# Kernel optimization log

Hardware: AMD Instinct MI355X
Metric: run time of the kernel (lower is better)

## Reference

```python
import jax, jax.numpy as jnp
import numpy as np
from jax import lax

B, S, I = 128, 256, 128          # batch, seq_len, input_size
CTX, OUT = 256, 128              # context_input_size, output_size
CPM, NM = 1024, 4                # center_size_per_module, num_modules
CENTER = NM * CPM
IN_SIZES = [I + CTX, CTX, CTX, CTX]          # only module 0 sees the input
HID = [CPM, CPM, CPM, CPM + OUT]             # last module also emits output


def setup_inputs() -> dict:
    key = jax.random.key(0)
    ks = jax.random.split(key, 4 + 5 * NM)
    d = {
        "inputs": jax.random.normal(ks[0], (B, 1, S, I), jnp.float32),
        "center_init": jax.random.normal(ks[1], (NM, B, CPM), jnp.float32),
        "mod_init": jax.random.normal(ks[2], (NM - 1, B, CPM), jnp.float32),
        "mod_init_last": jax.random.normal(ks[3], (B, CPM + OUT), jnp.float32),
    }
    for i in range(NM):
        k = ks[4 + 5 * i: 4 + 5 * (i + 1)]
        d[f"pm{i}"] = jax.random.normal(k[0], (CENTER, CTX), jnp.float32) * 0.02
        d[f"wih{i}"] = jax.random.normal(k[1], (3 * HID[i], IN_SIZES[i]), jnp.float32) * 0.05
        d[f"whh{i}"] = jax.random.normal(k[2], (3 * HID[i], HID[i]), jnp.float32) * 0.05
        d[f"bih{i}"] = jnp.zeros((3 * HID[i],), jnp.float32)
        d[f"bhh{i}"] = jnp.zeros((3 * HID[i],), jnp.float32)
    return d


def _gru(x, h, wih, whh, bih, bhh):
    # PyTorch GRUCell semantics
    gi = x @ wih.T + bih
    gh = h @ whh.T + bhh
    ir, iz, inn = jnp.split(gi, 3, axis=1)
    hr, hz, hn = jnp.split(gh, 3, axis=1)
    r = jax.nn.sigmoid(ir + hr)
    z = jax.nn.sigmoid(iz + hz)
    n = jnp.tanh(inn + r * hn)
    return (1.0 - z) * n + z * h


def _forward(inputs, center_init, mod_init, mod_init_last, pms, wihs, whhs, bihs, bhhs):
    xs = jnp.swapaxes(inputs[:, 0], 0, 1)  # [S, B, I]

    def step(carry, x_t):
        centers, mods, mod_last = carry  # [NM,B,CPM], [NM-1,B,CPM], [B,CPM+OUT]
        # torch.cat(prev_center_states, dim=1): module-major concat -> [B, NM*CPM]
        center_state = jnp.reshape(jnp.swapaxes(centers, 0, 1), (centers.shape[1], -1))
        new_centers, new_mods = [], []
        out = new_mod_last = None
        for i in range(NM):
            ctx = center_state @ pms[i]                       # [B, CTX]
            xin = jnp.concatenate([x_t, ctx], axis=1) if i == 0 else ctx
            h_prev = mod_last if i == NM - 1 else mods[i]
            h = _gru(xin, h_prev, wihs[i], whhs[i], bihs[i], bhhs[i])
            if i == NM - 1:
                out = h[:, :OUT]                              # split([output, center_feat])
                new_centers.append(h[:, OUT:])
                new_mod_last = h
            else:
                new_centers.append(h)
                new_mods.append(h)
        return (jnp.stack(new_centers), jnp.stack(new_mods), new_mod_last), out

    _, ys = lax.scan(step, (center_init, mod_init, mod_init_last), xs)
    return jnp.swapaxes(ys, 0, 1)  # [B, S, OUT]


def reference(inputs, center_init, mod_init, mod_init_last,
              pm0, pm1, pm2, pm3,
              wih0, wih1, wih2, wih3,
              whh0, whh1, whh2, whh3,
              bih0, bih1, bih2, bih3,
              bhh0, bhh1, bhh2, bhh3):
    return _forward(inputs, center_init, mod_init, mod_init_last,
                    (pm0, pm1, pm2, pm3),
                    (wih0, wih1, wih2, wih3),
                    (whh0, whh1, whh2, whh3),
                    (bih0, bih1, bih2, bih3),
                    (bhh0, bhh1, bhh2, bhh3))
```

## Files before the change

### kernel.cpp

```cpp
#include <hip/hip_runtime.h>
#include <hip/hip_bf16.h>

typedef _Float16 f16;
typedef f16  f16x8 __attribute__((ext_vector_type(8)));
typedef float f32x4 __attribute__((ext_vector_type(4)));

__device__ __forceinline__ f16x8 ld8h(const f16* p){ return *reinterpret_cast<const f16x8*>(p); }
__device__ __forceinline__ void fsplit(float x, f16* hi, f16* lo){
    f16 h=(f16)x; *hi=h; *lo=(f16)((x-(float)h)*4096.0f);
}
#define MFMA16(a,b,c) __builtin_amdgcn_mfma_f32_16x16x32_f16((a),(b),(c),0,0,0)
__device__ __forceinline__ size_t fragoff(int n, int k, int Kc){
    return ((size_t)(n>>4)*Kc + (k>>5))*512 + (size_t)((((k&31)>>3)*16 + (n&15))*8 + (k&7));
}

constexpr size_t NXE   = 128ull*256*128;
constexpr size_t NPM   = 1024ull*4096;
constexpr size_t NWIH0 = 3072ull*384;
constexpr size_t NWIH12= 3072ull*256;
constexpr size_t NWIH3 = 3456ull*256;
constexpr size_t NWHH  = 3072ull*1024;
constexpr size_t NWHH3 = 3456ull*1152;
constexpr size_t NCTX  = 128ull*1024;
constexpr size_t NHMX  = 128ull*1152;

constexpr size_t OFF_XH    = 0;
constexpr size_t OFF_XL    = OFF_XH + NXE*2;
constexpr size_t OFF_PMH   = OFF_XL + NXE*2;
constexpr size_t OFF_PML   = OFF_PMH + NPM*2;
constexpr size_t OFF_WIHH0 = OFF_PML + NPM*2;
constexpr size_t OFF_WIHH1 = OFF_WIHH0 + NWIH0*2;
constexpr size_t OFF_WIHH2 = OFF_WIHH1 + NWIH12*2;
constexpr size_t OFF_WIHH3 = OFF_WIHH2 + NWIH12*2;
constexpr size_t OFF_WIHL0 = OFF_WIHH3 + NWIH3*2;
constexpr size_t OFF_WIHL1 = OFF_WIHL0 + NWIH0*2;
constexpr size_t OFF_WIHL2 = OFF_WIHL1 + NWIH12*2;
constexpr size_t OFF_WIHL3 = OFF_WIHL2 + NWIH12*2;
constexpr size_t OFF_WHHH0 = OFF_WIHL3 + NWIH3*2;
constexpr size_t OFF_WHHH1 = OFF_WHHH0 + NWHH*2;
constexpr size_t OFF_WHHH2 = OFF_WHHH1 + NWHH*2;
constexpr size_t OFF_WHHH3 = OFF_WHHH2 + NWHH*2;
constexpr size_t OFF_WHHL0 = OFF_WHHH3 + NWHH3*2;
constexpr size_t OFF_WHHL1 = OFF_WHHL0 + NWHH*2;
constexpr size_t OFF_WHHL2 = OFF_WHHL1 + NWHH*2;
constexpr size_t OFF_WHHL3 = OFF_WHHL2 + NWHH*2;
constexpr size_t OFF_C0H   = OFF_WHHL3 + NWHH3*2;
constexpr size_t OFF_C0L   = OFF_C0H + 4*NHMX*2;
constexpr size_t OFF_CTXH  = OFF_C0L + 4*NHMX*2;
constexpr size_t OFF_CTXL  = OFF_CTXH + NCTX*2;
constexpr size_t OFF_HH    = OFF_CTXL + NCTX*2;
constexpr size_t OFF_HL    = OFF_HH + 8*NHMX*2;
constexpr size_t WS_NEED   = OFF_HL + 8*NHMX*2;

__device__ __forceinline__ f16* hh_ptr(char* ws,int p,int i){ return (f16*)(ws+OFF_HH+((size_t)(p*4+i))*NHMX*2); }
__device__ __forceinline__ f16* hl_ptr(char* ws,int p,int i){ return (f16*)(ws+OFF_HL+((size_t)(p*4+i))*NHMX*2); }

__global__ void k_repack_w(const float* __restrict__ src, f16* __restrict__ hi,
                           f16* __restrict__ lo, int K){
    int n = blockIdx.x;
    const float* row = src + (size_t)n*K;
    int Kc = K >> 5;
    for (int k8 = threadIdx.x*8; k8 < K; k8 += 2048) {
        f16x8 hv, lv;
        #pragma unroll
        for (int e = 0; e < 8; ++e) { f16 a,b; fsplit(row[k8+e], &a, &b); hv[e]=a; lv[e]=b; }
        size_t d = fragoff(n, k8, Kc);
        *reinterpret_cast<f16x8*>(hi + d) = hv;
        *reinterpret_cast<f16x8*>(lo + d) = lv;
    }
}

__global__ void k_repack_pm(const float* __restrict__ p0, const float* __restrict__ p1,
                            const float* __restrict__ p2, const float* __restrict__ p3,
                            f16* __restrict__ hi, f16* __restrict__ lo){
    int k0 = blockIdx.x * 8;
    for (int c = threadIdx.x; c < 1024; c += 256) {
        int i = c >> 8, nl = c & 255;
        const float* p = (i==0?p0 : i==1?p1 : i==2?p2 : p3);
        #pragma unroll
        for (int e = 0; e < 8; ++e) {
            f16 a,b; fsplit(p[(size_t)(k0+e)*256 + nl], &a, &b);
            size_t d = fragoff(c, k0+e, 128); hi[d]=a; lo[d]=b;
        }
    }
}

__global__ void k_repack_x(const float* __restrict__ src, f16* __restrict__ hi, f16* __restrict__ lo){
    size_t g = ((size_t)blockIdx.x*256 + threadIdx.x) * 8;
    if (g >= NXE) return;
    int m = (int)(g >> 15), t = (int)((g >> 7) & 255), d0 = (int)(g & 127);
    f16x8 hv, lv;
    #pragma unroll
    for (int e = 0; e < 8; ++e) { f16 a,b; fsplit(src[g+e], &a, &b); hv[e]=a; lv[e]=b; }
    size_t d = (size_t)t*16384 + fragoff(m, d0, 4);
    *reinterpret_cast<f16x8*>(hi + d) = hv;
    *reinterpret_cast<f16x8*>(lo + d) = lv;
}

__global__ void k_init_cen(const float* __restrict__ ci, char* ws){
    size_t g = ((size_t)blockIdx.x*256 + threadIdx.x) * 8;
    if (g >= 4ull*128*1024) return;
    int i = (int)(g >> 17), b = (int)((g >> 10) & 127), c = (int)(g & 1023);
    f16* hi = (f16*)(ws + OFF_C0H) + (size_t)i*NHMX;
    f16* lo = (f16*)(ws + OFF_C0L) + (size_t)i*NHMX;
    f16x8 hv, lv;
    #pragma unroll
    for (int e = 0; e < 8; ++e) { f16 a,bb; fsplit(ci[g+e], &a, &bb); hv[e]=a; lv[e]=bb; }
    size_t d = (i < 3) ? fragoff(b, c, 32) : fragoff(b, 128 + c, 36);
    *reinterpret_cast<f16x8*>(hi + d) = hv;
    *reinterpret_cast<f16x8*>(lo + d) = lv;
}

__global__ void k_init_mod(const float* __restrict__ mi, char* ws){
    size_t g = ((size_t)blockIdx.x*256 + threadIdx.x) * 8;
    if (g >= 3ull*128*1024) return;
    int i = (int)(g >> 17), b = (int)((g >> 10) & 127), j = (int)(g & 1023);
    f16 *hh = hh_ptr(ws, 0, i), *hl = hl_ptr(ws, 0, i);
    f16x8 hv, lv;
    #pragma unroll
    for (int e = 0; e < 8; ++e) { f16 a,bb; fsplit(mi[g+e], &a, &bb); hv[e]=a; lv[e]=bb; }
    size_t d = fragoff(b, j, 32);
    *reinterpret_cast<f16x8*>(hh + d) = hv;
    *reinterpret_cast<f16x8*>(hl + d) = lv;
}

__global__ void k_init_last(const float* __restrict__ ml, char* ws){
    int b = blockIdx.x;
    f16 *hh = hh_ptr(ws, 0, 3), *hl = hl_ptr(ws, 0, 3);
    for (int j = threadIdx.x*8; j < 1152; j += 2048) {
        f16x8 hv, lv;
        #pragma unroll
        for (int e = 0; e < 8; ++e) { f16 a,bb; fsplit(ml[(size_t)b*1152 + j + e], &a, &bb); hv[e]=a; lv[e]=bb; }
        size_t d = fragoff(b, j, 36);
        *reinterpret_cast<f16x8*>(hh + d) = hv;
        *reinterpret_cast<f16x8*>(hl + d) = lv;
    }
}

__global__ __launch_bounds__(512) void k_ctx(char* ws, int par, int t){
    __shared__ float red[8][32][17];
    const f16* pmh  = (const f16*)(ws + OFF_PMH);
    const f16* pml  = (const f16*)(ws + OFF_PML);
    int tid = threadIdx.x, lane = tid & 63, wv = tid >> 6;
    int bm = blockIdx.x >> 6, bn = blockIdx.x & 63;
    int mod = wv >> 1, half = wv & 1;
    const int Kc_m = (mod == 3) ? 36 : 32;
    const int koff = ((mod == 3) ? 4 : 0) + half*16;
    const f16 *Ah, *Al;
    if (t == 0) {
        Ah = (const f16*)(ws + OFF_C0H) + (size_t)mod*NHMX;
        Al = (const f16*)(ws + OFF_C0L) + (size_t)mod*NHMX;
    } else {
        Ah = hh_ptr(ws, par, mod);
        Al = hl_ptr(ws, par, mod);
    }
    size_t lb = (size_t)lane*8;
    size_t a0 = ((size_t)(bm*2)*Kc_m + koff)*512 + lb;
    size_t a1 = a0 + (size_t)Kc_m*512;
    size_t bb = ((size_t)bn*128 + wv*16)*512 + lb;
    f32x4 h0={},h1={},c0={},c1={};
    #pragma unroll 4
    for (int kc = 0; kc < 16; ++kc) {
        f16x8 bh = ld8h(pmh + bb + kc*512), bl = ld8h(pml + bb + kc*512);
        f16x8 ah0 = ld8h(Ah + a0 + kc*512), al0 = ld8h(Al + a0 + kc*512);
        f16x8 ah1 = ld8h(Ah + a1 + kc*512), al1 = ld8h(Al + a1 + kc*512);
        h0 = MFMA16(ah0,bh,h0); c0 = MFMA16(al0,bh,c0); c0 = MFMA16(ah0,bl,c0);
        h1 = MFMA16(ah1,bh,h1); c1 = MFMA16(al1,bh,c1); c1 = MFMA16(ah1,bl,c1);
    }
    int rg = lane >> 4, fr = lane & 15;
    const float inv = 1.0f/4096.0f;
    #pragma unroll
    for (int rr = 0; rr < 4; ++rr) {
        red[wv][rg*4+rr][fr]      = h0[rr] + c0[rr]*inv;
        red[wv][16+rg*4+rr][fr]   = h1[rr] + c1[rr]*inv;
    }
    __syncthreads();
    int r = tid >> 4, c = tid & 15;
    float s = red[0][r][c]+red[1][r][c]+red[2][r][c]+red[3][r][c]
            + red[4][r][c]+red[5][r][c]+red[6][r][c]+red[7][r][c];
    int m = bm*32 + r, n = bn*16 + c;
    size_t d = fragoff(m, n, 32);
    f16* ctxh = (f16*)(ws + OFF_CTXH);
    f16* ctxl = (f16*)(ws + OFF_CTXL);
    fsplit(s, &ctxh[d], &ctxl[d]);
}

__global__ __launch_bounds__(512, 2) void k_fused(char* ws,
    const float* __restrict__ bih0, const float* __restrict__ bih1,
    const float* __restrict__ bih2, const float* __restrict__ bih3,
    const float* __restrict__ bhh0, const float* __restrict__ bhh1,
    const float* __restrict__ bhh2, const float* __restrict__ bhh3,
    float* __restrict__ out, int t, int par)
{
    __shared__ float red[3][4][64][17];
    const int tid = threadIdx.x, lane = tid & 63, wv = tid >> 6;
    const int kq = wv & 3, mp = wv >> 2;
    const int fr = lane & 15, rg = lane >> 4;
    const int tile = blockIdx.x >> 1, rh = blockIdx.x & 1;
    int i, jt;
    if (tile < 64)       { i = 0; jt = tile; }
    else if (tile < 128) { i = 1; jt = tile - 64; }
    else if (tile < 192) { i = 2; jt = tile - 128; }
    else                 { i = 3; jt = tile - 192; }
    const int H  = (i == 3) ? 1152 : 1024;
    const int K1 = (i == 0) ? 384 : 256;
    const int Kc1 = K1 >> 5, KcH = H >> 5, Ht = H >> 4;
    const int P1q = Kc1 >> 2, PHq = KcH >> 2;

    const f16* WihH = (const f16*)(ws + (i==0?OFF_WIHH0 : i==1?OFF_WIHH1 : i==2?OFF_WIHH2 : OFF_WIHH3));
    const f16* WihL = (const f16*)(ws + (i==0?OFF_WIHL0 : i==1?OFF_WIHL1 : i==2?OFF_WIHL2 : OFF_WIHL3));
    const f16* WhhH = (const f16*)(ws + (i==0?OFF_WHHH0 : i==1?OFF_WHHH1 : i==2?OFF_WHHH2 : OFF_WHHH3));
    const f16* WhhL = (const f16*)(ws + (i==0?OFF_WHHL0 : i==1?OFF_WHHL1 : i==2?OFF_WHHL2 : OFF_WHHL3));

    const size_t lb = (size_t)lane*8;
    size_t b1[3], b2[3];
    #pragma unroll
    for (int s = 0; s < 3; ++s) {
        b1[s] = ((size_t)(s*Ht + jt)*Kc1)*512 + lb;
        b2[s] = ((size_t)(s*Ht + jt)*KcH)*512 + lb;
    }
    const int mt0 = rh*4 + mp*2;

    f32x4 aRh[2]={{},{}}, aRc[2]={{},{}}, aZh[2]={{},{}}, aZc[2]={{},{}};
    f32x4 aIh[2]={{},{}}, aIc[2]={{},{}}, aNh[2]={{},{}}, aNc[2]={{},{}};

    {
        const f16* XH_ = (const f16*)(ws + OFF_XH);
        const f16* XL_ = (const f16*)(ws + OFF_XL);
        const f16* CH_ = (const f16*)(ws + OFF_CTXH);
        const f16* CL_ = (const f16*)(ws + OFF_CTXL);
        size_t xb0 = ((size_t)(t*8 + mt0)*4)*512 + lb, xb1 = xb0 + 2048;
        size_t cb0 = ((size_t)mt0*32)*512 + lb,        cb1 = cb0 + 16384;
        const int kc0 = kq*P1q, kc1e = kc0 + P1q;
        #pragma unroll 2
        for (int kc = kc0; kc < kc1e; ++kc) {
            f16x8 ah0, al0, ah1, al1;
            if (i == 0 && kc < 4) {
                ah0 = ld8h(XH_ + xb0 + kc*512); al0 = ld8h(XL_ + xb0 + kc*512);
                ah1 = ld8h(XH_ + xb1 + kc*512); al1 = ld8h(XL_ + xb1 + kc*512);
            } else {
                const int ck = (i == 0) ? kc - 4 : i*8 + kc;
                ah0 = ld8h(CH_ + cb0 + ck*512); al0 = ld8h(CL_ + cb0 + ck*512);
                ah1 = ld8h(CH_ + cb1 + ck*512); al1 = ld8h(CL_ + cb1 + ck*512);
            }
            f16x8 bh, bl;
            bh = ld8h(WihH + b1[0] + kc*512); bl = ld8h(WihL + b1[0] + kc*512);
            aRh[0]=MFMA16(ah0,bh,aRh[0]); aRc[0]=MFMA16(al0,bh,aRc[0]); aRc[0]=MFMA16(ah0,bl,aRc[0]);
            aRh[1]=MFMA16(ah1,bh,aRh[1]); aRc[1]=MFMA16(al1,bh,aRc[1]); aRc[1]=MFMA16(ah1,bl,aRc[1]);
            bh = ld8h(WihH + b1[1] + kc*512); bl = ld8h(WihL + b1[1] + kc*512);
            aZh[0]=MFMA16(ah0,bh,aZh[0]); aZc[0]=MFMA16(al0,bh,aZc[0]); aZc[0]=MFMA16(ah0,bl,aZc[0]);
            aZh[1]=MFMA16(ah1,bh,aZh[1]); aZc[1]=MFMA16(al1,bh,aZc[1]); aZc[1]=MFMA16(ah1,bl,aZc[1]);
            bh = ld8h(WihH + b1[2] + kc*512); bl = ld8h(WihL + b1[2] + kc*512);
            aIh[0]=MFMA16(ah0,bh,aIh[0]); aIc[0]=MFMA16(al0,bh,aIc[0]); aIc[0]=MFMA16(ah0,bl,aIc[0]);
            aIh[1]=MFMA16(ah1,bh,aIh[1]); aIc[1]=MFMA16(al1,bh,aIc[1]); aIc[1]=MFMA16(ah1,bl,aIc[1]);
        }
    }
    {
        const f16* HHp = hh_ptr(ws, par, i);
        const f16* HLp = hl_ptr(ws, par, i);
        size_t hb0 = ((size_t)mt0*KcH)*512 + lb, hb1 = hb0 + (size_t)KcH*512;
        const int kc0 = kq*PHq, kc1e = kc0 + PHq;
        #pragma unroll 2
        for (int kc = kc0; kc < kc1e; ++kc) {
            f16x8 ah0 = ld8h(HHp + hb0 + kc*512), al0 = ld8h(HLp + hb0 + kc*512);
            f16x8 ah1 = ld8h(HHp + hb1 + kc*512), al1 = ld8h(HLp + hb1 + kc*512);
            f16x8 bh, bl;
            bh = ld8h(WhhH + b2[0] + kc*512); bl = ld8h(WhhL + b2[0] + kc*512);
            aRh[0]=MFMA16(ah0,bh,aRh[0]); aRc[0]=MFMA16(al0,bh,aRc[0]); aRc[0]=MFMA16(ah0,bl,aRc[0]);
            aRh[1]=MFMA16(ah1,bh,aRh[1]); aRc[1]=MFMA16(al1,bh,aRc[1]); aRc[1]=MFMA16(ah1,bl,aRc[1]);
            bh = ld8h(WhhH + b2[1] + kc*512); bl = ld8h(WhhL + b2[1] + kc*512);
            aZh[0]=MFMA16(ah0,bh,aZh[0]); aZc[0]=MFMA16(al0,bh,aZc[0]); aZc[0]=MFMA16(ah0,bl,aZc[0]);
            aZh[1]=MFMA16(ah1,bh,aZh[1]); aZc[1]=MFMA16(al1,bh,aZc[1]); aZc[1]=MFMA16(ah1,bl,aZc[1]);
            bh = ld8h(WhhH + b2[2] + kc*512); bl = ld8h(WhhL + b2[2] + kc*512);
            aNh[0]=MFMA16(ah0,bh,aNh[0]); aNc[0]=MFMA16(al0,bh,aNc[0]); aNc[0]=MFMA16(ah0,bl,aNc[0]);
            aNh[1]=MFMA16(ah1,bh,aNh[1]); aNc[1]=MFMA16(al1,bh,aNc[1]); aNc[1]=MFMA16(ah1,bl,aNc[1]);
        }
    }

    const float inv = 1.0f/4096.0f;
    const int r16 = rg*4;
    if (kq != 0) {
        #pragma unroll
        for (int mi = 0; mi < 2; ++mi) {
            #pragma unroll
            for (int rr = 0; rr < 4; ++rr) {
                const int row = mp*32 + mi*16 + r16 + rr;
                red[kq-1][0][row][fr] = aRh[mi][rr] + aRc[mi][rr]*inv;
                red[kq-1][1][row][fr] = aZh[mi][rr] + aZc[mi][rr]*inv;
                red[kq-1][2][row][fr] = aIh[mi][rr] + aIc[mi][rr]*inv;
                red[kq-1][3][row][fr] = aNh[mi][rr] + aNc[mi][rr]*inv;
            }
        }
    }
    __syncthreads();
    if (kq != 0) return;

    const float* bihp = (i==0?bih0 : i==1?bih1 : i==2?bih2 : bih3);
    const float* bhhp = (i==0?bhh0 : i==1?bhh1 : i==2?bhh2 : bhh3);
    const int j = jt*16 + fr;
    const float bir = bihp[j], biz = bihp[H+j], bin = bihp[2*H+j];
    const float bhr = bhhp[j], bhz = bhhp[H+j], bhn = bhhp[2*H+j];
    const f16* hhP = hh_ptr(ws, par, i);
    const f16* hlP = hl_ptr(ws, par, i);
    f16 *hhN = hh_ptr(ws, par^1, i), *hlN = hl_ptr(ws, par^1, i);
    #pragma unroll
    for (int mi = 0; mi < 2; ++mi) {
        #pragma unroll
        for (int rr = 0; rr < 4; ++rr) {
            const int row = mp*32 + mi*16 + r16 + rr;
            float r_  = aRh[mi][rr] + aRc[mi][rr]*inv
                      + red[0][0][row][fr] + red[1][0][row][fr] + red[2][0][row][fr] + bir + bhr;
            float z_  = aZh[mi][rr] + aZc[mi][rr]*inv
                      + red[0][1][row][fr] + red[1][1][row][fr] + red[2][1][row][fr] + biz + bhz;
            float in_ = aIh[mi][rr] + aIc[mi][rr]*inv
                      + red[0][2][row][fr] + red[1][2][row][fr] + red[2][2][row][fr] + bin;
            float hn_ = aNh[mi][rr] + aNc[mi][rr]*inv
                      + red[0][3][row][fr] + red[1][3][row][fr] + red[2][3][row][fr] + bhn;
            float rgt = 1.f/(1.f + expf(-r_));
            float zgt = 1.f/(1.f + expf(-z_));
            float ngt = tanhf(in_ + rgt*hn_);
            const int m = rh*64 + row;
            size_t hd = fragoff(m, j, KcH);
            float hp = (float)hhP[hd] + (float)hlP[hd]*inv;
            float hnew = (1.f - zgt)*ngt + zgt*hp;
            fsplit(hnew, &hhN[hd], &hlN[hd]);
            if (i == 3 && j < 128)
                out[((size_t)m*256 + t)*128 + j] = hnew;
        }
    }
}

extern "C" void kernel_launch(void* const* d_in, const int* in_sizes, int n_in,
                              void* d_out, int out_size, void* d_ws, size_t ws_size,
                              hipStream_t stream)
{
    char* ws = (char*)d_ws;
    const float* inp   = (const float*)d_in[0];
    const float* cini  = (const float*)d_in[1];
    const float* mini  = (const float*)d_in[2];
    const float* mlast = (const float*)d_in[3];
    const float *pm[4], *wih[4], *whh[4], *bih[4], *bhh[4];
    for (int i = 0; i < 4; ++i) {
        pm[i]  = (const float*)d_in[4 + 5*i];
        wih[i] = (const float*)d_in[5 + 5*i];
        whh[i] = (const float*)d_in[6 + 5*i];
        bih[i] = (const float*)d_in[7 + 5*i];
        bhh[i] = (const float*)d_in[8 + 5*i];
    }
    float* out = (float*)d_out;

    k_repack_x<<<2048, 256, 0, stream>>>(inp, (f16*)(ws+OFF_XH), (f16*)(ws+OFF_XL));
    k_repack_pm<<<512, 256, 0, stream>>>(pm[0], pm[1], pm[2], pm[3],
                                         (f16*)(ws+OFF_PMH), (f16*)(ws+OFF_PML));
    k_repack_w<<<3072, 256, 0, stream>>>(wih[0], (f16*)(ws+OFF_WIHH0), (f16*)(ws+OFF_WIHL0), 384);
    k_repack_w<<<3072, 256, 0, stream>>>(wih[1], (f16*)(ws+OFF_WIHH1), (f16*)(ws+OFF_WIHL1), 256);
    k_repack_w<<<3072, 256, 0, stream>>>(wih[2], (f16*)(ws+OFF_WIHH2), (f16*)(ws+OFF_WIHL2), 256);
    k_repack_w<<<3456, 256, 0, stream>>>(wih[3], (f16*)(ws+OFF_WIHH3), (f16*)(ws+OFF_WIHL3), 256);
    k_repack_w<<<3072, 256, 0, stream>>>(whh[0], (f16*)(ws+OFF_WHHH0), (f16*)(ws+OFF_WHHL0), 1024);
    k_repack_w<<<3072, 256, 0, stream>>>(whh[1], (f16*)(ws+OFF_WHHH1), (f16*)(ws+OFF_WHHL1), 1024);
    k_repack_w<<<3072, 256, 0, stream>>>(whh[2], (f16*)(ws+OFF_WHHH2), (f16*)(ws+OFF_WHHL2), 1024);
    k_repack_w<<<3456, 256, 0, stream>>>(whh[3], (f16*)(ws+OFF_WHHH3), (f16*)(ws+OFF_WHHL3), 1152);
    k_init_cen<<<256, 256, 0, stream>>>(cini, ws);
    k_init_mod<<<192, 256, 0, stream>>>(mini, ws);
    k_init_last<<<128, 256, 0, stream>>>(mlast, ws);

    for (int t = 0; t < 256; ++t) {
        int par = t & 1;
        k_ctx<<<256, 512, 0, stream>>>(ws, par, t);
        k_fused<<<528, 512, 0, stream>>>(ws,
            bih[0], bih[1], bih[2], bih[3],
            bhh[0], bhh[1], bhh[2], bhh[3],
            out, t, par);
    }
    (void)in_sizes; (void)n_in; (void)out_size; (void)ws_size; (void)WS_NEED;
}
```

Before: 12.58 ms.

## Run recurrent W_hh GEMM concurrently with context GEMM in one launch

The recurrent h@W_hh^T product no longer depends on the context, so it moves into a combined kernel that runs alongside the context GEMM blocks. Its gate pre-activations are written to a new global scratch buffer. A second kernel then computes only the input-side GEMM and the GRU elementwise update, reading those values back. The aim is to shorten the serial critical path per timestep and use more CUs at once, at the cost of an extra global round trip for the gate values and a reworked tile schedule with blocks interleaved by stride 66.

After: 13.66 ms. 1.09x slower.

```diff
diff --git a/kernel.cpp b/kernel.cpp
--- a/kernel.cpp
+++ b/kernel.cpp
@@ -50,7 +50,8 @@
 constexpr size_t OFF_CTXL  = OFF_CTXH + NCTX*2;
 constexpr size_t OFF_HH    = OFF_CTXL + NCTX*2;
 constexpr size_t OFF_HL    = OFF_HH + 8*NHMX*2;
-constexpr size_t WS_NEED   = OFF_HL + 8*NHMX*2;
+constexpr size_t OFF_G2    = OFF_HL + 8*NHMX*2;
+constexpr size_t WS_NEED   = OFF_G2 + 528ull*3*1024*4;
 
 __device__ __forceinline__ f16* hh_ptr(char* ws,int p,int i){ return (f16*)(ws+OFF_HH+((size_t)(p*4+i))*NHMX*2); }
 __device__ __forceinline__ f16* hl_ptr(char* ws,int p,int i){ return (f16*)(ws+OFF_HL+((size_t)(p*4+i))*NHMX*2); }
@@ -137,66 +138,147 @@
     }
 }
 
-__global__ __launch_bounds__(512) void k_ctx(char* ws, int par, int t){
-    __shared__ float red[8][32][17];
-    const f16* pmh  = (const f16*)(ws + OFF_PMH);
-    const f16* pml  = (const f16*)(ws + OFF_PML);
-    int tid = threadIdx.x, lane = tid & 63, wv = tid >> 6;
-    int bm = blockIdx.x >> 6, bn = blockIdx.x & 63;
-    int mod = wv >> 1, half = wv & 1;
-    const int Kc_m = (mod == 3) ? 36 : 32;
-    const int koff = ((mod == 3) ? 4 : 0) + half*16;
-    const f16 *Ah, *Al;
-    if (t == 0) {
-        Ah = (const f16*)(ws + OFF_C0H) + (size_t)mod*NHMX;
-        Al = (const f16*)(ws + OFF_C0L) + (size_t)mod*NHMX;
-    } else {
-        Ah = hh_ptr(ws, par, mod);
-        Al = hl_ptr(ws, par, mod);
-    }
-    size_t lb = (size_t)lane*8;
-    size_t a0 = ((size_t)(bm*2)*Kc_m + koff)*512 + lb;
-    size_t a1 = a0 + (size_t)Kc_m*512;
-    size_t bb = ((size_t)bn*128 + wv*16)*512 + lb;
-    f32x4 h0={},h1={},c0={},c1={};
-    #pragma unroll 4
-    for (int kc = 0; kc < 16; ++kc) {
-        f16x8 bh = ld8h(pmh + bb + kc*512), bl = ld8h(pml + bb + kc*512);
-        f16x8 ah0 = ld8h(Ah + a0 + kc*512), al0 = ld8h(Al + a0 + kc*512);
-        f16x8 ah1 = ld8h(Ah + a1 + kc*512), al1 = ld8h(Al + a1 + kc*512);
-        h0 = MFMA16(ah0,bh,h0); c0 = MFMA16(al0,bh,c0); c0 = MFMA16(ah0,bl,c0);
-        h1 = MFMA16(ah1,bh,h1); c1 = MFMA16(al1,bh,c1); c1 = MFMA16(ah1,bl,c1);
-    }
-    int rg = lane >> 4, fr = lane & 15;
+__global__ __launch_bounds__(512, 2) void k_union(char* ws, int t, int par)
+{
+    __shared__ float smem[9792];
+    const int tid = threadIdx.x, lane = tid & 63, wv = tid >> 6;
+    const int fr = lane & 15, rg = lane >> 4;
+    const size_t lb = (size_t)lane*8;
     const float inv = 1.0f/4096.0f;
-    #pragma unroll
-    for (int rr = 0; rr < 4; ++rr) {
-        red[wv][rg*4+rr][fr]      = h0[rr] + c0[rr]*inv;
-        red[wv][16+rg*4+rr][fr]   = h1[rr] + c1[rr]*inv;
+
+    if (blockIdx.x < 256) {
+        float (*red)[32][17] = (float(*)[32][17])smem;
+        const f16* pmh  = (const f16*)(ws + OFF_PMH);
+        const f16* pml  = (const f16*)(ws + OFF_PML);
+        int bm = blockIdx.x >> 6, bn = blockIdx.x & 63;
+        int mod = wv >> 1, half = wv & 1;
+        const int Kc_m = (mod == 3) ? 36 : 32;
+        const int koff = ((mod == 3) ? 4 : 0) + half*16;
+        const f16 *Ah, *Al;
+        if (t == 0) {
+            Ah = (const f16*)(ws + OFF_C0H) + (size_t)mod*NHMX;
+            Al = (const f16*)(ws + OFF_C0L) + (size_t)mod*NHMX;
+        } else {
+            Ah = hh_ptr(ws, par, mod);
+            Al = hl_ptr(ws, par, mod);
+        }
+        size_t a0 = ((size_t)(bm*2)*Kc_m + koff)*512 + lb;
+        size_t a1 = a0 + (size_t)Kc_m*512;
+        size_t bb = ((size_t)bn*128 + wv*16)*512 + lb;
+        f32x4 h0={},h1={},c0={},c1={};
+        #pragma unroll 4
+        for (int kc = 0; kc < 16; ++kc) {
+            f16x8 bh = ld8h(pmh + bb + kc*512), bl = ld8h(pml + bb + kc*512);
+            f16x8 ah0 = ld8h(Ah + a0 + kc*512), al0 = ld8h(Al + a0 + kc*512);
+            f16x8 ah1 = ld8h(Ah + a1 + kc*512), al1 = ld8h(Al + a1 + kc*512);
+            h0 = MFMA16(ah0,bh,h0); c0 = MFMA16(al0,bh,c0); c0 = MFMA16(ah0,bl,c0);
+            h1 = MFMA16(ah1,bh,h1); c1 = MFMA16(al1,bh,c1); c1 = MFMA16(ah1,bl,c1);
+        }
+        #pragma unroll
+        for (int rr = 0; rr < 4; ++rr) {
+            red[wv][rg*4+rr][fr]    = h0[rr] + c0[rr]*inv;
+            red[wv][16+rg*4+rr][fr] = h1[rr] + c1[rr]*inv;
+        }
+        __syncthreads();
+        int r = tid >> 4, c = tid & 15;
+        float s = red[0][r][c]+red[1][r][c]+red[2][r][c]+red[3][r][c]
+                + red[4][r][c]+red[5][r][c]+red[6][r][c]+red[7][r][c];
+        int m = bm*32 + r, n = bn*16 + c;
+        size_t d = fragoff(m, n, 32);
+        f16* ctxh = (f16*)(ws + OFF_CTXH);
+        f16* ctxl = (f16*)(ws + OFF_CTXL);
+        fsplit(s, &ctxh[d], &ctxl[d]);
+        return;
+    }
+
+    float (*red)[3][64][17] = (float(*)[3][64][17])smem;
+    const int hid = blockIdx.x - 256;
+    const int lid = (hid & 7)*66 + (hid >> 3);
+    const int tile = lid >> 1, rh = lid & 1;
+    int i, jt;
+    if (tile < 64)       { i = 0; jt = tile; }
+    else if (tile < 128) { i = 1; jt = tile - 64; }
+    else if (tile < 192) { i = 2; jt = tile - 128; }
+    else                 { i = 3; jt = tile - 192; }
+    const int H  = (i == 3) ? 1152 : 1024;
+    const int KcH = H >> 5, Ht = H >> 4;
+    const int PHq = KcH >> 2;
+
+    const f16* WhhH = (const f16*)(ws + (i==0?OFF_WHHH0 : i==1?OFF_WHHH1 : i==2?OFF_WHHH2 : OFF_WHHH3));
+    const f16* WhhL = (const f16*)(ws + (i==0?OFF_WHHL0 : i==1?OFF_WHHL1 : i==2?OFF_WHHL2 : OFF_WHHL3));
+    size_t b2[3];
+    #pragma unroll
+    for (int s = 0; s < 3; ++s) b2[s] = ((size_t)(s*Ht + jt)*KcH)*512 + lb;
+
+    const int kq = wv & 3, mp = wv >> 2;
+    const int mt0 = rh*4 + mp*2;
+    f32x4 aRh[2]={{},{}}, aRc[2]={{},{}}, aZh[2]={{},{}}, aZc[2]={{},{}};
+    f32x4 aNh[2]={{},{}}, aNc[2]={{},{}};
+
+    const f16* HHp = hh_ptr(ws, par, i);
+    const f16* HLp = hl_ptr(ws, par, i);
+    size_t hb0 = ((size_t)mt0*KcH)*512 + lb, hb1 = hb0 + (size_t)KcH*512;
+    const int kc0 = kq*PHq, kc1e = kc0 + PHq;
+    #pragma unroll 2
+    for (int kc = kc0; kc < kc1e; ++kc) {
+        f16x8 ah0 = ld8h(HHp + hb0 + kc*512), al0 = ld8h(HLp + hb0 + kc*512);
+        f16x8 ah1 = ld8h(HHp + hb1 + kc*512), al1 = ld8h(HLp + hb1 + kc*512);
+        f16x8 bh, bl;
+        bh = ld8h(WhhH + b2[0] + kc*512); bl = ld8h(WhhL + b2[0] + kc*512);
+        aRh[0]=MFMA16(ah0,bh,aRh[0]); aRc[0]=MFMA16(al0,bh,aRc[0]); aRc[0]=MFMA16(ah0,bl,aRc[0]);
+        aRh[1]=MFMA16(ah1,bh,aRh[1]); aRc[1]=MFMA16(al1,bh,aRc[1]); aRc[1]=MFMA16(ah1,bl,aRc[1]);
+        bh = ld8h(WhhH + b2[1] + kc*512); bl = ld8h(WhhL + b2[1] + kc*512);
+        aZh[0]=MFMA16(ah0,bh,aZh[0]); aZc[0]=MFMA16(al0,bh,aZc[0]); aZc[0]=MFMA16(ah0,bl,aZc[0]);
+        aZh[1]=MFMA16(ah1,bh,aZh[1]); aZc[1]=MFMA16(al1,bh,aZc[1]); aZc[1]=MFMA16(ah1,bl,aZc[1]);
+        bh = ld8h(WhhH + b2[2] + kc*512); bl = ld8h(WhhL + b2[2] + kc*512);
+        aNh[0]=MFMA16(ah0,bh,aNh[0]); aNc[0]=MFMA16(al0,bh,aNc[0]); aNc[0]=MFMA16(ah0,bl,aNc[0]);
+        aNh[1]=MFMA16(ah1,bh,aNh[1]); aNc[1]=MFMA16(al1,bh,aNc[1]); aNc[1]=MFMA16(ah1,bl,aNc[1]);
+    }
+
+    const int r16 = rg*4;
+    if (kq != 0) {
+        #pragma unroll
+        for (int mi = 0; mi < 2; ++mi) {
+            #pragma unroll
+            for (int rr = 0; rr < 4; ++rr) {
+                const int row = mp*32 + mi*16 + r16 + rr;
+                red[kq-1][0][row][fr] = aRh[mi][rr] + aRc[mi][rr]*inv;
+                red[kq-1][1][row][fr] = aZh[mi][rr] + aZc[mi][rr]*inv;
+                red[kq-1][2][row][fr] = aNh[mi][rr] + aNc[mi][rr]*inv;
+            }
+        }
     }
     __syncthreads();
-    int r = tid >> 4, c = tid & 15;
-    float s = red[0][r][c]+red[1][r][c]+red[2][r][c]+red[3][r][c]
-            + red[4][r][c]+red[5][r][c]+red[6][r][c]+red[7][r][c];
-    int m = bm*32 + r, n = bn*16 + c;
-    size_t d = fragoff(m, n, 32);
-    f16* ctxh = (f16*)(ws + OFF_CTXH);
-    f16* ctxl = (f16*)(ws + OFF_CTXL);
-    fsplit(s, &ctxh[d], &ctxl[d]);
-}
-
-__global__ __launch_bounds__(512, 2) void k_fused(char* ws,
+    if (kq != 0) return;
+
+    float* G2 = (float*)(ws + OFF_G2) + (size_t)lid*3*1024;
+    #pragma unroll
+    for (int mi = 0; mi < 2; ++mi) {
+        #pragma unroll
+        for (int rr = 0; rr < 4; ++rr) {
+            const int row = mp*32 + mi*16 + r16 + rr;
+            float R = aRh[mi][rr] + aRc[mi][rr]*inv + red[0][0][row][fr] + red[1][0][row][fr] + red[2][0][row][fr];
+            float Z = aZh[mi][rr] + aZc[mi][rr]*inv + red[0][1][row][fr] + red[1][1][row][fr] + red[2][1][row][fr];
+            float N = aNh[mi][rr] + aNc[mi][rr]*inv + red[0][2][row][fr] + red[1][2][row][fr] + red[2][2][row][fr];
+            G2[0*1024 + row*16 + fr] = R;
+            G2[1*1024 + row*16 + fr] = Z;
+            G2[2*1024 + row*16 + fr] = N;
+        }
+    }
+}
+
+__global__ __launch_bounds__(256, 2) void k_rest(char* ws,
     const float* __restrict__ bih0, const float* __restrict__ bih1,
     const float* __restrict__ bih2, const float* __restrict__ bih3,
     const float* __restrict__ bhh0, const float* __restrict__ bhh1,
     const float* __restrict__ bhh2, const float* __restrict__ bhh3,
     float* __restrict__ out, int t, int par)
 {
-    __shared__ float red[3][4][64][17];
-    const int tid = threadIdx.x, lane = tid & 63, wv = tid >> 6;
-    const int kq = wv & 3, mp = wv >> 2;
+    __shared__ float red[3][3][64][17];
+    const int tid = threadIdx.x, lane = tid & 63, kq = tid >> 6;
     const int fr = lane & 15, rg = lane >> 4;
-    const int tile = blockIdx.x >> 1, rh = blockIdx.x & 1;
+    const int lid = (blockIdx.x & 7)*66 + (blockIdx.x >> 3);
+    const int tile = lid >> 1, rh = lid & 1;
     int i, jt;
     if (tile < 64)       { i = 0; jt = tile; }
     else if (tile < 128) { i = 1; jt = tile - 64; }
@@ -204,76 +286,58 @@
     else                 { i = 3; jt = tile - 192; }
     const int H  = (i == 3) ? 1152 : 1024;
     const int K1 = (i == 0) ? 384 : 256;
-    const int Kc1 = K1 >> 5, KcH = H >> 5, Ht = H >> 4;
-    const int P1q = Kc1 >> 2, PHq = KcH >> 2;
+    const int Kc1 = K1 >> 5, Ht = H >> 4;
+    const int KcH = H >> 5;
+    const int P1q = Kc1 >> 2;
 
     const f16* WihH = (const f16*)(ws + (i==0?OFF_WIHH0 : i==1?OFF_WIHH1 : i==2?OFF_WIHH2 : OFF_WIHH3));
     const f16* WihL = (const f16*)(ws + (i==0?OFF_WIHL0 : i==1?OFF_WIHL1 : i==2?OFF_WIHL2 : OFF_WIHL3));
-    const f16* WhhH = (const f16*)(ws + (i==0?OFF_WHHH0 : i==1?OFF_WHHH1 : i==2?OFF_WHHH2 : OFF_WHHH3));
-    const f16* WhhL = (const f16*)(ws + (i==0?OFF_WHHL0 : i==1?OFF_WHHL1 : i==2?OFF_WHHL2 : OFF_WHHL3));
-
     const size_t lb = (size_t)lane*8;
-    size_t b1[3], b2[3];
-    #pragma unroll
-    for (int s = 0; s < 3; ++s) {
-        b1[s] = ((size_t)(s*Ht + jt)*Kc1)*512 + lb;
-        b2[s] = ((size_t)(s*Ht + jt)*KcH)*512 + lb;
-    }
-    const int mt0 = rh*4 + mp*2;
-
-    f32x4 aRh[2]={{},{}}, aRc[2]={{},{}}, aZh[2]={{},{}}, aZc[2]={{},{}};
-    f32x4 aIh[2]={{},{}}, aIc[2]={{},{}}, aNh[2]={{},{}}, aNc[2]={{},{}};
+    size_t b1[3];
+    #pragma unroll
+    for (int s = 0; s < 3; ++s) b1[s] = ((size_t)(s*Ht + jt)*Kc1)*512 + lb;
+    const int mt0 = rh*4;
+
+    f32x4 aRh[4]={}, aRc[4]={}, aZh[4]={}, aZc[4]={}, aIh[4]={}, aIc[4]={};
 
     {
         const f16* XH_ = (const f16*)(ws + OFF_XH);
         const f16* XL_ = (const f16*)(ws + OFF_XL);
         const f16* CH_ = (const f16*)(ws + OFF_CTXH);
         const f16* CL_ = (const f16*)(ws + OFF_CTXL);
-        size_t xb0 = ((size_t)(t*8 + mt0)*4)*512 + lb, xb1 = xb0 + 2048;
-        size_t cb0 = ((size_t)mt0*32)*512 + lb,        cb1 = cb0 + 16384;
+        size_t xb[4], cb[4];
+        #pragma unroll
+        for (int f = 0; f < 4; ++f) {
+            xb[f] = ((size_t)(t*8 + mt0 + f)*4)*512 + lb;
+            cb[f] = ((size_t)(mt0 + f)*32)*512 + lb;
+        }
         const int kc0 = kq*P1q, kc1e = kc0 + P1q;
-        #pragma unroll 2
         for (int kc = kc0; kc < kc1e; ++kc) {
-            f16x8 ah0, al0, ah1, al1;
+            f16x8 ah[4], al[4];
             if (i == 0 && kc < 4) {
-                ah0 = ld8h(XH_ + xb0 + kc*512); al0 = ld8h(XL_ + xb0 + kc*512);
-                ah1 = ld8h(XH_ + xb1 + kc*512); al1 = ld8h(XL_ + xb1 + kc*512);
+                #pragma unroll
+                for (int f = 0; f < 4; ++f) { ah[f] = ld8h(XH_ + xb[f] + kc*512); al[f] = ld8h(XL_ + xb[f] + kc*512); }
             } else {
                 const int ck = (i == 0) ? kc - 4 : i*8 + kc;
-                ah0 = ld8h(CH_ + cb0 + ck*512); al0 = ld8h(CL_ + cb0 + ck*512);
-                ah1 = ld8h(CH_ + cb1 + ck*512); al1 = ld8h(CL_ + cb1 + ck*512);
+                #pragma unroll
+                for (int f = 0; f < 4; ++f) { ah[f] = ld8h(CH_ + cb[f] + ck*512); al[f] = ld8h(CL_ + cb[f] + ck*512); }
             }
             f16x8 bh, bl;
             bh = ld8h(WihH + b1[0] + kc*512); bl = ld8h(WihL + b1[0] + kc*512);
-            aRh[0]=MFMA16(ah0,bh,aRh[0]); aRc[0]=MFMA16(al0,bh,aRc[0]); aRc[0]=MFMA16(ah0,bl,aRc[0]);
-            aRh[1]=MFMA16(ah1,bh,aRh[1]); aRc[1]=MFMA16(al1,bh,aRc[1]); aRc[1]=MFMA16(ah1,bl,aRc[1]);
+            #pragma unroll
+            for (int f = 0; f < 4; ++f) {
+                aRh[f]=MFMA16(ah[f],bh,aRh[f]); aRc[f]=MFMA16(al[f],bh,aRc[f]); aRc[f]=MFMA16(ah[f],bl,aRc[f]);
+            }
             bh = ld8h(WihH + b1[1] + kc*512); bl = ld8h(WihL + b1[1] + kc*512);
-            aZh[0]=MFMA16(ah0,bh,aZh[0]); aZc[0]=MFMA16(al0,bh,aZc[0]); aZc[0]=MFMA16(ah0,bl,aZc[0]);
-            aZh[1]=MFMA16(ah1,bh,aZh[1]); aZc[1]=MFMA16(al1,bh,aZc[1]); aZc[1]=MFMA16(ah1,bl,aZc[1]);
+            #pragma unroll
+            for (int f = 0; f < 4; ++f) {
+                aZh[f]=MFMA16(ah[f],bh,aZh[f]); aZc[f]=MFMA16(al[f],bh,aZc[f]); aZc[f]=MFMA16(ah[f],bl,aZc[f]);
+            }
             bh = ld8h(WihH + b1[2] + kc*512); bl = ld8h(WihL + b1[2] + kc*512);
-            aIh[0]=MFMA16(ah0,bh,aIh[0]); aIc[0]=MFMA16(al0,bh,aIc[0]); aIc[0]=MFMA16(ah0,bl,aIc[0]);
-            aIh[1]=MFMA16(ah1,bh,aIh[1]); aIc[1]=MFMA16(al1,bh,aIc[1]); aIc[1]=MFMA16(ah1,bl,aIc[1]);
-        }
-    }
-    {
-        const f16* HHp = hh_ptr(ws, par, i);
-        const f16* HLp = hl_ptr(ws, par, i);
-        size_t hb0 = ((size_t)mt0*KcH)*512 + lb, hb1 = hb0 + (size_t)KcH*512;
-        const int kc0 = kq*PHq, kc1e = kc0 + PHq;
-        #pragma unroll 2
-        for (int kc = kc0; kc < kc1e; ++kc) {
-            f16x8 ah0 = ld8h(HHp + hb0 + kc*512), al0 = ld8h(HLp + hb0 + kc*512);
-            f16x8 ah1 = ld8h(HHp + hb1 + kc*512), al1 = ld8h(HLp + hb1 + kc*512);
-            f16x8 bh, bl;
-            bh = ld8h(WhhH + b2[0] + kc*512); bl = ld8h(WhhL + b2[0] + kc*512);
-            aRh[0]=MFMA16(ah0,bh,aRh[0]); aRc[0]=MFMA16(al0,bh,aRc[0]); aRc[0]=MFMA16(ah0,bl,aRc[0]);
-            aRh[1]=MFMA16(ah1,bh,aRh[1]); aRc[1]=MFMA16(al1,bh,aRc[1]); aRc[1]=MFMA16(ah1,bl,aRc[1]);
-            bh = ld8h(WhhH + b2[1] + kc*512); bl = ld8h(WhhL + b2[1] + kc*512);
-            aZh[0]=MFMA16(ah0,bh,aZh[0]); aZc[0]=MFMA16(al0,bh,aZc[0]); aZc[0]=MFMA16(ah0,bl,aZc[0]);
-            aZh[1]=MFMA16(ah1,bh,aZh[1]); aZc[1]=MFMA16(al1,bh,aZc[1]); aZc[1]=MFMA16(ah1,bl,aZc[1]);
-            bh = ld8h(WhhH + b2[2] + kc*512); bl = ld8h(WhhL + b2[2] + kc*512);
-            aNh[0]=MFMA16(ah0,bh,aNh[0]); aNc[0]=MFMA16(al0,bh,aNc[0]); aNc[0]=MFMA16(ah0,bl,aNc[0]);
-            aNh[1]=MFMA16(ah1,bh,aNh[1]); aNc[1]=MFMA16(al1,bh,aNc[1]); aNc[1]=MFMA16(ah1,bl,aNc[1]);
+            #pragma unroll
+            for (int f = 0; f < 4; ++f) {
+                aIh[f]=MFMA16(ah[f],bh,aIh[f]); aIc[f]=MFMA16(al[f],bh,aIc[f]); aIc[f]=MFMA16(ah[f],bl,aIc[f]);
+            }
         }
     }
 
@@ -281,14 +345,13 @@
     const int r16 = rg*4;
     if (kq != 0) {
         #pragma unroll
-        for (int mi = 0; mi < 2; ++mi) {
+        for (int mi = 0; mi < 4; ++mi) {
             #pragma unroll
             for (int rr = 0; rr < 4; ++rr) {
-                const int row = mp*32 + mi*16 + r16 + rr;
+                const int row = mi*16 + r16 + rr;
                 red[kq-1][0][row][fr] = aRh[mi][rr] + aRc[mi][rr]*inv;
                 red[kq-1][1][row][fr] = aZh[mi][rr] + aZc[mi][rr]*inv;
                 red[kq-1][2][row][fr] = aIh[mi][rr] + aIc[mi][rr]*inv;
-                red[kq-1][3][row][fr] = aNh[mi][rr] + aNc[mi][rr]*inv;
             }
         }
     }
@@ -303,19 +366,25 @@
     const f16* hhP = hh_ptr(ws, par, i);
     const f16* hlP = hl_ptr(ws, par, i);
     f16 *hhN = hh_ptr(ws, par^1, i), *hlN = hl_ptr(ws, par^1, i);
-    #pragma unroll
-    for (int mi = 0; mi < 2; ++mi) {
+    const float* G2 = (const float*)(ws + OFF_G2) + (size_t)lid*3*1024;
+    #pragma unroll
+    for (int mi = 0; mi < 4; ++mi) {
         #pragma unroll
         for (int rr = 0; rr < 4; ++rr) {
-            const int row = mp*32 + mi*16 + r16 + rr;
-            float r_  = aRh[mi][rr] + aRc[mi][rr]*inv
-                      + red[0][0][row][fr] + red[1][0][row][fr] + red[2][0][row][fr] + bir + bhr;
-            float z_  = aZh[mi][rr] + aZc[mi][rr]*inv
-                      + red[0][1][row][fr] + red[1][1][row][fr] + red[2][1][row][fr] + biz + bhz;
-            float in_ = aIh[mi][rr] + aIc[mi][rr]*inv
-                      + red[0][2][row][fr] + red[1][2][row][fr] + red[2][2][row][fr] + bin;
-            float hn_ = aNh[mi][rr] + aNc[mi][rr]*inv
-                      + red[0][3][row][fr] + red[1][3][row][fr] + red[2][3][row][fr] + bhn;
+            const int row = mi*16 + r16 + rr;
+            float ihR = aRh[mi][rr] + aRc[mi][rr]*inv
+                      + red[0][0][row][fr] + red[1][0][row][fr] + red[2][0][row][fr];
+            float ihZ = aZh[mi][rr] + aZc[mi][rr]*inv
+                      + red[0][1][row][fr] + red[1][1][row][fr] + red[2][1][row][fr];
+            float ihI = aIh[mi][rr] + aIc[mi][rr]*inv
+                      + red[0][2][row][fr] + red[1][2][row][fr] + red[2][2][row][fr];
+            float hhR = G2[0*1024 + row*16 + fr];
+            float hhZ = G2[1*1024 + row*16 + fr];
+            float hhN_ = G2[2*1024 + row*16 + fr];
+            float r_  = ihR + hhR + bir + bhr;
+            float z_  = ihZ + hhZ + biz + bhz;
+            float in_ = ihI + bin;
+            float hn_ = hhN_ + bhn;
             float rgt = 1.f/(1.f + expf(-r_));
             float zgt = 1.f/(1.f + expf(-z_));
             float ngt = tanhf(in_ + rgt*hn_);
@@ -366,8 +435,8 @@
 
     for (int t = 0; t < 256; ++t) {
         int par = t & 1;
-        k_ctx<<<256, 512, 0, stream>>>(ws, par, t);
-        k_fused<<<528, 512, 0, stream>>>(ws,
+        k_union<<<784, 512, 0, stream>>>(ws, t, par);
+        k_rest<<<528, 256, 0, stream>>>(ws,
             bih[0], bih[1], bih[2], bih[3],
             bhh[0], bhh[1], bhh[2], bhh[3],
             out, t, par);
```

## Stage GRU weight tiles through LDS with async double buffering, drop split-K

Applied to the files above, without the earlier changes.

The fused GRU-step kernel now uses 256 threads per block, with each wave owning one 16-row batch tile over the full K range. This removes the split-K reduction through shared memory. Weight fragments for each K-chunk are loaded once per block into a double-buffered LDS tile with global_load_lds and shared across all four waves, instead of each wave reading them from global memory. Block indices are also remapped so neighbouring blocks land on different XCD-like groups. In exchange, each wave does a longer serial K loop with a barrier per chunk and fewer waves per block.

After: 21.73 ms. 1.73x slower.

```diff
diff --git a/kernel.cpp b/kernel.cpp
--- a/kernel.cpp
+++ b/kernel.cpp
@@ -12,6 +12,11 @@
 #define MFMA16(a,b,c) __builtin_amdgcn_mfma_f32_16x16x32_f16((a),(b),(c),0,0,0)
 __device__ __forceinline__ size_t fragoff(int n, int k, int Kc){
     return ((size_t)(n>>4)*Kc + (k>>5))*512 + (size_t)((((k&31)>>3)*16 + (n&15))*8 + (k&7));
+}
+__device__ __forceinline__ void gl_lds16(const f16* g, f16* l){
+    __builtin_amdgcn_global_load_lds(
+        (const __attribute__((address_space(1))) void*)g,
+        (__attribute__((address_space(3))) void*)l, 16, 0, 0);
 }
 
 constexpr size_t NXE   = 128ull*256*128;
@@ -185,18 +190,18 @@
     fsplit(s, &ctxh[d], &ctxl[d]);
 }
 
-__global__ __launch_bounds__(512, 2) void k_fused(char* ws,
+__global__ __launch_bounds__(256, 2) void k_fused(char* ws,
     const float* __restrict__ bih0, const float* __restrict__ bih1,
     const float* __restrict__ bih2, const float* __restrict__ bih3,
     const float* __restrict__ bhh0, const float* __restrict__ bhh1,
     const float* __restrict__ bhh2, const float* __restrict__ bhh3,
     float* __restrict__ out, int t, int par)
 {
-    __shared__ float red[3][4][64][17];
+    __shared__ f16 Bs[2][24][512];
     const int tid = threadIdx.x, lane = tid & 63, wv = tid >> 6;
-    const int kq = wv & 3, mp = wv >> 2;
     const int fr = lane & 15, rg = lane >> 4;
-    const int tile = blockIdx.x >> 1, rh = blockIdx.x & 1;
+    const int lid = (blockIdx.x & 7)*66 + (blockIdx.x >> 3);
+    const int tile = lid >> 1, rh = lid & 1;
     int i, jt;
     if (tile < 64)       { i = 0; jt = tile; }
     else if (tile < 128) { i = 1; jt = tile - 64; }
@@ -205,128 +210,116 @@
     const int H  = (i == 3) ? 1152 : 1024;
     const int K1 = (i == 0) ? 384 : 256;
     const int Kc1 = K1 >> 5, KcH = H >> 5, Ht = H >> 4;
-    const int P1q = Kc1 >> 2, PHq = KcH >> 2;
+    const int P1 = Kc1 >> 2, PH = KcH >> 2, P = P1 + PH;
 
     const f16* WihH = (const f16*)(ws + (i==0?OFF_WIHH0 : i==1?OFF_WIHH1 : i==2?OFF_WIHH2 : OFF_WIHH3));
     const f16* WihL = (const f16*)(ws + (i==0?OFF_WIHL0 : i==1?OFF_WIHL1 : i==2?OFF_WIHL2 : OFF_WIHL3));
     const f16* WhhH = (const f16*)(ws + (i==0?OFF_WHHH0 : i==1?OFF_WHHH1 : i==2?OFF_WHHH2 : OFF_WHHH3));
     const f16* WhhL = (const f16*)(ws + (i==0?OFF_WHHL0 : i==1?OFF_WHHL1 : i==2?OFF_WHHL2 : OFF_WHHL3));
 
+    size_t b1[3], b2[3];
+    #pragma unroll
+    for (int s = 0; s < 3; ++s) {
+        b1[s] = ((size_t)(s*Ht + jt)*Kc1)*512;
+        b2[s] = ((size_t)(s*Ht + jt)*KcH)*512;
+    }
+    const int mf = rh*4 + wv;
     const size_t lb = (size_t)lane*8;
-    size_t b1[3], b2[3];
-    #pragma unroll
-    for (int s = 0; s < 3; ++s) {
-        b1[s] = ((size_t)(s*Ht + jt)*Kc1)*512 + lb;
-        b2[s] = ((size_t)(s*Ht + jt)*KcH)*512 + lb;
-    }
-    const int mt0 = rh*4 + mp*2;
-
-    f32x4 aRh[2]={{},{}}, aRc[2]={{},{}}, aZh[2]={{},{}}, aZc[2]={{},{}};
-    f32x4 aIh[2]={{},{}}, aIc[2]={{},{}}, aNh[2]={{},{}}, aNc[2]={{},{}};
-
-    {
-        const f16* XH_ = (const f16*)(ws + OFF_XH);
-        const f16* XL_ = (const f16*)(ws + OFF_XL);
-        const f16* CH_ = (const f16*)(ws + OFF_CTXH);
-        const f16* CL_ = (const f16*)(ws + OFF_CTXL);
-        size_t xb0 = ((size_t)(t*8 + mt0)*4)*512 + lb, xb1 = xb0 + 2048;
-        size_t cb0 = ((size_t)mt0*32)*512 + lb,        cb1 = cb0 + 16384;
-        const int kc0 = kq*P1q, kc1e = kc0 + P1q;
-        #pragma unroll 2
-        for (int kc = kc0; kc < kc1e; ++kc) {
-            f16x8 ah0, al0, ah1, al1;
-            if (i == 0 && kc < 4) {
-                ah0 = ld8h(XH_ + xb0 + kc*512); al0 = ld8h(XL_ + xb0 + kc*512);
-                ah1 = ld8h(XH_ + xb1 + kc*512); al1 = ld8h(XL_ + xb1 + kc*512);
-            } else {
-                const int ck = (i == 0) ? kc - 4 : i*8 + kc;
-                ah0 = ld8h(CH_ + cb0 + ck*512); al0 = ld8h(CL_ + cb0 + ck*512);
-                ah1 = ld8h(CH_ + cb1 + ck*512); al1 = ld8h(CL_ + cb1 + ck*512);
-            }
+
+    const f16* XH_ = (const f16*)(ws + OFF_XH);
+    const f16* XL_ = (const f16*)(ws + OFF_XL);
+    const f16* CH_ = (const f16*)(ws + OFF_CTXH);
+    const f16* CL_ = (const f16*)(ws + OFF_CTXL);
+    const f16* HHp = hh_ptr(ws, par, i);
+    const f16* HLp = hl_ptr(ws, par, i);
+    const size_t xb = ((size_t)(t*8 + mf)*4)*512 + lb;
+    const size_t cb = ((size_t)mf*32)*512 + lb;
+    const size_t hb = ((size_t)mf*KcH)*512 + lb;
+
+    f32x4 aRh={}, aRc={}, aZh={}, aZc={}, aIh={}, aIc={}, aNh={}, aNc={};
+
+    auto stage = [&](int p){
+        const int buf = p & 1;
+        const bool ih = p < P1;
+        const int lp = ih ? p : p - P1;
+        #pragma unroll
+        for (int q = 0; q < 6; ++q) {
+            const int c = wv*6 + q;
+            const int s = c >> 3, a = (c >> 2) & 1, kc = c & 3;
+            const f16* base = ih ? (a ? WihL : WihH) : (a ? WhhL : WhhH);
+            const size_t off = (ih ? b1[s] : b2[s]) + (size_t)(lp*4 + kc)*512 + lb;
+            gl_lds16(base + off, &Bs[buf][c][0]);
+        }
+    };
+
+    auto computeIH = [&](int p){
+        const int buf = p & 1;
+        #pragma unroll
+        for (int kc = 0; kc < 4; ++kc) {
+            const int kcg = p*4 + kc;
+            f16x8 ah, al;
+            if (i == 0 && kcg < 4) { ah = ld8h(XH_ + xb + kcg*512); al = ld8h(XL_ + xb + kcg*512); }
+            else { const int ck = (i == 0) ? kcg - 4 : i*8 + kcg;
+                   ah = ld8h(CH_ + cb + ck*512); al = ld8h(CL_ + cb + ck*512); }
+            const f16* bp = &Bs[buf][kc][0] + lb;
             f16x8 bh, bl;
-            bh = ld8h(WihH + b1[0] + kc*512); bl = ld8h(WihL + b1[0] + kc*512);
-            aRh[0]=MFMA16(ah0,bh,aRh[0]); aRc[0]=MFMA16(al0,bh,aRc[0]); aRc[0]=MFMA16(ah0,bl,aRc[0]);
-            aRh[1]=MFMA16(ah1,bh,aRh[1]); aRc[1]=MFMA16(al1,bh,aRc[1]); aRc[1]=MFMA16(ah1,bl,aRc[1]);
-            bh = ld8h(WihH + b1[1] + kc*512); bl = ld8h(WihL + b1[1] + kc*512);
-            aZh[0]=MFMA16(ah0,bh,aZh[0]); aZc[0]=MFMA16(al0,bh,aZc[0]); aZc[0]=MFMA16(ah0,bl,aZc[0]);
-            aZh[1]=MFMA16(ah1,bh,aZh[1]); aZc[1]=MFMA16(al1,bh,aZc[1]); aZc[1]=MFMA16(ah1,bl,aZc[1]);
-            bh = ld8h(WihH + b1[2] + kc*512); bl = ld8h(WihL + b1[2] + kc*512);
-            aIh[0]=MFMA16(ah0,bh,aIh[0]); aIc[0]=MFMA16(al0,bh,aIc[0]); aIc[0]=MFMA16(ah0,bl,aIc[0]);
-            aIh[1]=MFMA16(ah1,bh,aIh[1]); aIc[1]=MFMA16(al1,bh,aIc[1]); aIc[1]=MFMA16(ah1,bl,aIc[1]);
+            bh = *(const f16x8*)(bp);            bl = *(const f16x8*)(bp + 2048);
+            aRh = MFMA16(ah,bh,aRh); aRc = MFMA16(al,bh,aRc); aRc = MFMA16(ah,bl,aRc);
+            bh = *(const f16x8*)(bp + 4096);     bl = *(const f16x8*)(bp + 6144);
+            aZh = MFMA16(ah,bh,aZh); aZc = MFMA16(al,bh,aZc); aZc = MFMA16(ah,bl,aZc);
+            bh = *(const f16x8*)(bp + 8192);     bl = *(const f16x8*)(bp + 10240);
+            aIh = MFMA16(ah,bh,aIh); aIc = MFMA16(al,bh,aIc); aIc = MFMA16(ah,bl,aIc);
         }
-    }
-    {
-        const f16* HHp = hh_ptr(ws, par, i);
-        const f16* HLp = hl_ptr(ws, par, i);
-        size_t hb0 = ((size_t)mt0*KcH)*512 + lb, hb1 = hb0 + (size_t)KcH*512;
-        const int kc0 = kq*PHq, kc1e = kc0 + PHq;
-        #pragma unroll 2
-        for (int kc = kc0; kc < kc1e; ++kc) {
-            f16x8 ah0 = ld8h(HHp + hb0 + kc*512), al0 = ld8h(HLp + hb0 + kc*512);
-            f16x8 ah1 = ld8h(HHp + hb1 + kc*512), al1 = ld8h(HLp + hb1 + kc*512);
+    };
+    auto computeHH = [&](int p){
+        const int buf = p & 1;
+        const int lp = p - P1;
+        #pragma unroll
+        for (int kc = 0; kc < 4; ++kc) {
+            const int kcg = lp*4 + kc;
+            f16x8 ah = ld8h(HHp + hb + kcg*512), al = ld8h(HLp + hb + kcg*512);
+            const f16* bp = &Bs[buf][kc][0] + lb;
             f16x8 bh, bl;
-            bh = ld8h(WhhH + b2[0] + kc*512); bl = ld8h(WhhL + b2[0] + kc*512);
-            aRh[0]=MFMA16(ah0,bh,aRh[0]); aRc[0]=MFMA16(al0,bh,aRc[0]); aRc[0]=MFMA16(ah0,bl,aRc[0]);
-            aRh[1]=MFMA16(ah1,bh,aRh[1]); aRc[1]=MFMA16(al1,bh,aRc[1]); aRc[1]=MFMA16(ah1,bl,aRc[1]);
-            bh = ld8h(WhhH + b2[1] + kc*512); bl = ld8h(WhhL + b2[1] + kc*512);
-            aZh[0]=MFMA16(ah0,bh,aZh[0]); aZc[0]=MFMA16(al0,bh,aZc[0]); aZc[0]=MFMA16(ah0,bl,aZc[0]);
-            aZh[1]=MFMA16(ah1,bh,aZh[1]); aZc[1]=MFMA16(al1,bh,aZc[1]); aZc[1]=MFMA16(ah1,bl,aZc[1]);
-            bh = ld8h(WhhH + b2[2] + kc*512); bl = ld8h(WhhL + b2[2] + kc*512);
-            aNh[0]=MFMA16(ah0,bh,aNh[0]); aNc[0]=MFMA16(al0,bh,aNc[0]); aNc[0]=MFMA16(ah0,bl,aNc[0]);
-            aNh[1]=MFMA16(ah1,bh,aNh[1]); aNc[1]=MFMA16(al1,bh,aNc[1]); aNc[1]=MFMA16(ah1,bl,aNc[1]);
+            bh = *(const f16x8*)(bp);            bl = *(const f16x8*)(bp + 2048);
+            aRh = MFMA16(ah,bh,aRh); aRc = MFMA16(al,bh,aRc); aRc = MFMA16(ah,bl,aRc);
+            bh = *(const f16x8*)(bp + 4096);     bl = *(const f16x8*)(bp + 6144);
+            aZh = MFMA16(ah,bh,aZh); aZc = MFMA16(al,bh,aZc); aZc = MFMA16(ah,bl,aZc);
+            bh = *(const f16x8*)(bp + 8192);     bl = *(const f16x8*)(bp + 10240);
+            aNh = MFMA16(ah,bh,aNh); aNc = MFMA16(al,bh,aNc); aNc = MFMA16(ah,bl,aNc);
         }
+    };
+
+    stage(0);
+    __syncthreads();
+    for (int p = 0; p < P; ++p) {
+        if (p + 1 < P) stage(p + 1);
+        if (p < P1) computeIH(p); else computeHH(p);
+        __syncthreads();
     }
 
     const float inv = 1.0f/4096.0f;
-    const int r16 = rg*4;
-    if (kq != 0) {
-        #pragma unroll
-        for (int mi = 0; mi < 2; ++mi) {
-            #pragma unroll
-            for (int rr = 0; rr < 4; ++rr) {
-                const int row = mp*32 + mi*16 + r16 + rr;
-                red[kq-1][0][row][fr] = aRh[mi][rr] + aRc[mi][rr]*inv;
-                red[kq-1][1][row][fr] = aZh[mi][rr] + aZc[mi][rr]*inv;
-                red[kq-1][2][row][fr] = aIh[mi][rr] + aIc[mi][rr]*inv;
-                red[kq-1][3][row][fr] = aNh[mi][rr] + aNc[mi][rr]*inv;
-            }
-        }
-    }
-    __syncthreads();
-    if (kq != 0) return;
-
     const float* bihp = (i==0?bih0 : i==1?bih1 : i==2?bih2 : bih3);
     const float* bhhp = (i==0?bhh0 : i==1?bhh1 : i==2?bhh2 : bhh3);
     const int j = jt*16 + fr;
     const float bir = bihp[j], biz = bihp[H+j], bin = bihp[2*H+j];
     const float bhr = bhhp[j], bhz = bhhp[H+j], bhn = bhhp[2*H+j];
-    const f16* hhP = hh_ptr(ws, par, i);
-    const f16* hlP = hl_ptr(ws, par, i);
     f16 *hhN = hh_ptr(ws, par^1, i), *hlN = hl_ptr(ws, par^1, i);
     #pragma unroll
-    for (int mi = 0; mi < 2; ++mi) {
-        #pragma unroll
-        for (int rr = 0; rr < 4; ++rr) {
-            const int row = mp*32 + mi*16 + r16 + rr;
-            float r_  = aRh[mi][rr] + aRc[mi][rr]*inv
-                      + red[0][0][row][fr] + red[1][0][row][fr] + red[2][0][row][fr] + bir + bhr;
-            float z_  = aZh[mi][rr] + aZc[mi][rr]*inv
-                      + red[0][1][row][fr] + red[1][1][row][fr] + red[2][1][row][fr] + biz + bhz;
-            float in_ = aIh[mi][rr] + aIc[mi][rr]*inv
-                      + red[0][2][row][fr] + red[1][2][row][fr] + red[2][2][row][fr] + bin;
-            float hn_ = aNh[mi][rr] + aNc[mi][rr]*inv
-                      + red[0][3][row][fr] + red[1][3][row][fr] + red[2][3][row][fr] + bhn;
-            float rgt = 1.f/(1.f + expf(-r_));
-            float zgt = 1.f/(1.f + expf(-z_));
-            float ngt = tanhf(in_ + rgt*hn_);
-            const int m = rh*64 + row;
-            size_t hd = fragoff(m, j, KcH);
-            float hp = (float)hhP[hd] + (float)hlP[hd]*inv;
-            float hnew = (1.f - zgt)*ngt + zgt*hp;
-            fsplit(hnew, &hhN[hd], &hlN[hd]);
-            if (i == 3 && j < 128)
-                out[((size_t)m*256 + t)*128 + j] = hnew;
-        }
+    for (int rr = 0; rr < 4; ++rr) {
+        float r_  = aRh[rr] + aRc[rr]*inv + bir + bhr;
+        float z_  = aZh[rr] + aZc[rr]*inv + biz + bhz;
+        float in_ = aIh[rr] + aIc[rr]*inv + bin;
+        float hn_ = aNh[rr] + aNc[rr]*inv + bhn;
+        float rgt = 1.f/(1.f + expf(-r_));
+        float zgt = 1.f/(1.f + expf(-z_));
+        float ngt = tanhf(in_ + rgt*hn_);
+        const int m = mf*16 + rg*4 + rr;
+        size_t hd = fragoff(m, j, KcH);
+        float hp = (float)HHp[hd] + (float)HLp[hd]*inv;
+        float hnew = (1.f - zgt)*ngt + zgt*hp;
+        fsplit(hnew, &hhN[hd], &hlN[hd]);
+        if (i == 3 && j < 128)
+            out[((size_t)m*256 + t)*128 + j] = hnew;
     }
 }
 
@@ -367,7 +360,7 @@
     for (int t = 0; t < 256; ++t) {
         int par = t & 1;
         k_ctx<<<256, 512, 0, stream>>>(ws, par, t);
-        k_fused<<<528, 512, 0, stream>>>(ws,
+        k_fused<<<528, 256, 0, stream>>>(ws,
             bih[0], bih[1], bih[2], bih[3],
             bhh[0], bhh[1], bhh[2], bhh[3],
             out, t, par);
```
